# Kernel optimization log

Measured on AMD Instinct MI355X. Metric: run time of the kernel, lower is better.

Reference implementation:

```python
import jax, jax.numpy as jnp
import numpy as np

D_MODEL, N_LAYERS, D_INNER, D_STATE, D_CONV, DT_RANK, NUM_CLASSES = 256, 4, 512, 16, 4, 16, 10
B, L = 8, 1024


def setup_inputs() -> dict:
    key = jax.random.key(0)
    ks = jax.random.split(key, 16)
    s = 0.02
    inp = {}
    inp['x'] = jax.random.normal(ks[0], (B, L, 1), jnp.float32)
    inp['input_w'] = jax.random.normal(ks[1], (D_MODEL, 1), jnp.float32) * s
    inp['input_b'] = jnp.zeros((D_MODEL,), jnp.float32)
    inp['ln_w'] = jnp.ones((N_LAYERS, D_MODEL), jnp.float32)
    inp['ln_b'] = jnp.zeros((N_LAYERS, D_MODEL), jnp.float32)
    inp['in_proj_w'] = jax.random.normal(ks[2], (N_LAYERS, 2 * D_INNER, D_MODEL), jnp.float32) * s
    inp['in_proj_b'] = jnp.zeros((N_LAYERS, 2 * D_INNER), jnp.float32)
    inp['conv_w'] = jax.random.normal(ks[3], (N_LAYERS, D_INNER, 1, D_CONV), jnp.float32) * 0.2
    inp['conv_b'] = jnp.zeros((N_LAYERS, D_INNER), jnp.float32)
    inp['x_proj_w'] = jax.random.normal(ks[4], (N_LAYERS, DT_RANK + 2 * D_STATE, D_INNER), jnp.float32) * s
    inp['dt_proj_w'] = jax.random.normal(ks[5], (N_LAYERS, D_INNER, DT_RANK), jnp.float32) * s
    inp['dt_proj_b'] = jax.random.normal(ks[6], (N_LAYERS, D_INNER), jnp.float32) * 0.1 - 4.0  # small softplus(dt)
    # canonical S4D-real init: A = [1..d_state] repeated over d_inner
    A = jnp.tile(jnp.arange(1, D_STATE + 1, dtype=jnp.float32)[None, :], (D_INNER, 1))
    inp['A_log'] = jnp.tile(jnp.log(A)[None], (N_LAYERS, 1, 1))
    inp['D'] = jnp.ones((N_LAYERS, D_INNER), jnp.float32)
    inp['out_proj_w'] = jax.random.normal(ks[7], (N_LAYERS, D_MODEL, D_INNER), jnp.float32) * s
    inp['out_proj_b'] = jnp.zeros((N_LAYERS, D_MODEL), jnp.float32)
    inp['norm_w'] = jnp.ones((D_MODEL,), jnp.float32)
    inp['norm_b'] = jnp.zeros((D_MODEL,), jnp.float32)
    inp['cls_w'] = jax.random.normal(ks[8], (NUM_CLASSES, D_MODEL), jnp.float32) * s
    inp['cls_b'] = jnp.zeros((NUM_CLASSES,), jnp.float32)
    return inp


def _layernorm(x, w, b, eps=1e-5):
    mu = jnp.mean(x, axis=-1, keepdims=True)
    var = jnp.mean(jnp.square(x - mu), axis=-1, keepdims=True)
    return (x - mu) * jax.lax.rsqrt(var + eps) * w + b


def _causal_depthwise_conv(u, w, b):
    # u: (B, L, D_inner), w: (D_inner, 1, K), causal padding K-1
    out = jax.lax.conv_general_dilated(
        u.transpose(0, 2, 1), w, window_strides=(1,), padding=[(D_CONV - 1, 0)],
        feature_group_count=D_INNER, dimension_numbers=('NCH', 'OIH', 'NCH'))
    return out.transpose(0, 2, 1) + b


def _selective_scan(u, delta, A, Bm, Cm, Dp):
    # u, delta: (B,L,Din); Bm, Cm: (B,L,N); A: (Din,N); Dp: (Din,)
    def step(h, inp):
        d_t, B_t, C_t, u_t = inp                       # (B,Din),(B,N),(B,N),(B,Din)
        dA = jnp.exp(d_t[:, :, None] * A)              # (B,Din,N)
        dBu = d_t[:, :, None] * B_t[:, None, :] * u_t[:, :, None]
        h = dA * h + dBu
        y = jnp.einsum('bdn,bn->bd', h, C_t)
        return h, y
    h0 = jnp.zeros((u.shape[0], D_INNER, D_STATE), u.dtype)
    xs = (delta.transpose(1, 0, 2), Bm.transpose(1, 0, 2), Cm.transpose(1, 0, 2), u.transpose(1, 0, 2))
    _, ys = jax.lax.scan(step, h0, xs)                 # ys: (L,B,Din)
    return ys.transpose(1, 0, 2) + u * Dp


def _mamba_layer(x, ln_w, ln_b, ipw, ipb, cw, cb, xpw, dtw, dtb, A_log, Dp, opw, opb):
    h = _layernorm(x, ln_w, ln_b)
    xz = jnp.einsum('bld,ed->ble', h, ipw) + ipb       # (B,L,2*Din)
    u, res = jnp.split(xz, 2, axis=-1)
    u = jax.nn.silu(_causal_depthwise_conv(u, cw, cb))
    x_dbl = jnp.einsum('bld,ed->ble', u, xpw)          # (B,L,dt_rank+2N)
    dt, Bm, Cm = jnp.split(x_dbl, [DT_RANK, DT_RANK + D_STATE], axis=-1)
    delta = jax.nn.softplus(jnp.einsum('blr,dr->bld', dt, dtw) + dtb)
    A = -jnp.exp(A_log)
    y = _selective_scan(u, delta, A, Bm, Cm, Dp)
    y = y * jax.nn.silu(res)
    return x + jnp.einsum('ble,de->bld', y, opw) + opb


def reference(x, input_w, input_b, ln_w, ln_b, in_proj_w, in_proj_b, conv_w, conv_b,
              x_proj_w, dt_proj_w, dt_proj_b, A_log, D, out_proj_w, out_proj_b,
              norm_w, norm_b, cls_w, cls_b):
    h = jnp.einsum('blc,dc->bld', x, input_w) + input_b   # (B,L,D_MODEL)
    for i in range(N_LAYERS):
        h = _mamba_layer(h, ln_w[i], ln_b[i], in_proj_w[i], in_proj_b[i], conv_w[i], conv_b[i],
                         x_proj_w[i], dt_proj_w[i], dt_proj_b[i], A_log[i], D[i],
                         out_proj_w[i], out_proj_b[i])
    h = _layernorm(h, norm_w, norm_b)
    pooled = jnp.mean(h, axis=1)                          # (B, D_MODEL)
    return jnp.einsum('bd,cd->bc', pooled, cls_w) + cls_b
```

## Files before the change

### kernel.cpp

```cpp
#include <hip/hip_runtime.h>
#include <hip/hip_bf16.h>
#include <math.h>

#define DM 256
#define NL 4
#define DI 512
#define DS 16
#define DC 4
#define DR 16
#define NC 10
#define NB 8
#define LL 1024
#define MR (NB*LL)
#define NCHUNK 64
#define CLEN 16

typedef __attribute__((ext_vector_type(4))) float f32x4;
typedef __attribute__((ext_vector_type(8))) short short8;

__device__ __forceinline__ float silu_f(float x) {
    return x * (1.0f / (1.0f + __expf(-x)));
}
__device__ __forceinline__ float bf2f(ushort v) {
    union { unsigned u; float f; } c; c.u = ((unsigned)v) << 16; return c.f;
}
__device__ __forceinline__ ushort f2bf(float f) {
    union { float f; unsigned u; } c; c.f = f;
    unsigned lsb = (c.u >> 16) & 1;
    return (ushort)((c.u + 0x7fffu + lsb) >> 16);
}
__device__ __forceinline__ void g2lds16(const void* g, void* l) {
    __builtin_amdgcn_global_load_lds((const __attribute__((address_space(1))) void*)g,
                                     (__attribute__((address_space(3))) void*)l, 16, 0, 0);
}

#define IPW_N (NL*2*DI*DM)
#define XPW_N (NL*64*DI)
#define OPW_N (NL*DM*DI)
__global__ __launch_bounds__(256) void convert_weights_kernel(
        const float* __restrict__ ipw, const float* __restrict__ xpw,
        const float* __restrict__ opw,
        ushort* __restrict__ ipw_b, ushort* __restrict__ xpw_b, ushort* __restrict__ opw_b) {
    int t = blockIdx.x * 256 + threadIdx.x;
    if (t < IPW_N) { ipw_b[t] = f2bf(ipw[t]); return; }
    t -= IPW_N;
    if (t < XPW_N) {
        int l = t >> 15, r = (t >> 9) & 63, k = t & 511;
        xpw_b[t] = (r < 48) ? f2bf(xpw[((size_t)l * 48 + r) * DI + k]) : (ushort)0;
        return;
    }
    t -= XPW_N;
    if (t < OPW_N) opw_b[t] = f2bf(opw[t]);
}

__global__ void input_proj_kernel(const float* __restrict__ x, const float* __restrict__ w,
                                  const float* __restrict__ b, float* __restrict__ h) {
    int t = blockIdx.x * 256 + threadIdx.x;
    if (t >= MR * DM) return;
    int d = t & (DM - 1);
    int m = t >> 8;
    h[t] = x[m] * w[d] + b[d];
}

__global__ __launch_bounds__(256) void layernorm_bf16_kernel(const float* __restrict__ in,
        const float* __restrict__ w, const float* __restrict__ b, ushort* __restrict__ out) {
    int row = blockIdx.x, t = threadIdx.x;
    float v = in[row * DM + t];
    float s = v, q = v * v;
#pragma unroll
    for (int o = 32; o >= 1; o >>= 1) { s += __shfl_xor(s, o); q += __shfl_xor(q, o); }
    __shared__ float red[8];
    int wid = t >> 6;
    if ((t & 63) == 0) { red[wid] = s; red[4 + wid] = q; }
    __syncthreads();
    s = red[0] + red[1] + red[2] + red[3];
    q = red[4] + red[5] + red[6] + red[7];
    float mu = s * (1.0f / DM);
    float var = q * (1.0f / DM) - mu * mu;
    float rs = rsqrtf(var + 1e-5f);
    out[row * DM + t] = f2bf((v - mu) * rs * w[t] + b[t]);
}

template<int BM, int BN, int WM, int WN, int MODE>
__global__ __launch_bounds__(256) void mfma_gemm_kernel(
        const ushort* __restrict__ A, int lda,
        const ushort* __restrict__ W,
        const float* __restrict__ bias,
        ushort* __restrict__ Cb, float* __restrict__ Cf, int ldc, int K) {
    constexpr int FM = BM / WM / 16;
    constexpr int FN = BN / WN / 16;
    __shared__ __align__(16) char smem[(BM + BN) * 128];
    const int tid = threadIdx.x;
    const int l = tid & 63, w = tid >> 6;
    const int wr = w / WN, wc = w % WN;
    const int bm = blockIdx.x * BM, bn = blockIdx.y * BN;
    const int ldw = K;

    f32x4 acc[FM][FN] = {};

    for (int k0 = 0; k0 < K; k0 += 64) {
#pragma unroll
        for (int i = 0; i < (BM * 128 / 16) / 256; i++) {
            int lin = (i * 256 + tid) * 16;
            int q = lin ^ (((lin >> 7) & 7) << 4);
            g2lds16(A + (size_t)(bm + (q >> 7)) * lda + k0 + ((q & 127) >> 1), smem + lin);
        }
#pragma unroll
        for (int i = 0; i < (BN * 128 / 16) / 256; i++) {
            int lin = (i * 256 + tid) * 16;
            int q = lin ^ (((lin >> 7) & 7) << 4);
            g2lds16(W + (size_t)(bn + (q >> 7)) * ldw + k0 + ((q & 127) >> 1),
                    smem + BM * 128 + lin);
        }
        __syncthreads();
        const int rl = l & 15;
        const int kb0 = ((l >> 4) << 3) * 2;
#pragma unroll
        for (int kk = 0; kk < 2; kk++) {
            short8 af[FM], bfr[FN];
#pragma unroll
            for (int m = 0; m < FM; m++) {
                int off = (wr * (BM / WM) + m * 16 + rl) * 128 + kk * 64 + kb0;
                off ^= ((off >> 7) & 7) << 4;
                af[m] = *(const short8*)(smem + off);
            }
#pragma unroll
            for (int n = 0; n < FN; n++) {
                int off = (wc * (BN / WN) + n * 16 + rl) * 128 + kk * 64 + kb0;
                off ^= ((off >> 7) & 7) << 4;
                bfr[n] = *(const short8*)(smem + BM * 128 + off);
            }
#pragma unroll
            for (int m = 0; m < FM; m++)
#pragma unroll
                for (int n = 0; n < FN; n++)
                    acc[m][n] = __builtin_amdgcn_mfma_f32_16x16x32_bf16(
                        af[m], bfr[n], acc[m][n], 0, 0, 0);
        }
        __syncthreads();
    }

    const int row0 = bm + wr * (BM / WM) + ((l >> 4) << 2);
    const int col0 = bn + wc * (BN / WN) + (l & 15);
#pragma unroll
    for (int m = 0; m < FM; m++) {
#pragma unroll
        for (int n = 0; n < FN; n++) {
            int col = col0 + n * 16;
            float bv = (MODE == 1) ? 0.f : bias[col];
#pragma unroll
            for (int r = 0; r < 4; r++) {
                size_t idx = (size_t)(row0 + m * 16 + r) * ldc + col;
                float v = acc[m][n][r];
                if (MODE == 0) Cb[idx] = f2bf(v + bv);
                else if (MODE == 1) Cf[idx] = v;
                else Cf[idx] += v + bv;
            }
        }
    }
}

__global__ __launch_bounds__(256) void conv_silu_kernel(const ushort* __restrict__ xz,
        const float* __restrict__ cw, const float* __restrict__ cb, ushort* __restrict__ u) {
    int t = blockIdx.x * 256 + threadIdx.x;
    int d8 = (t & 63) << 3;
    int m = t >> 6;
    int l = m & (LL - 1);
    const short8 zr = {0, 0, 0, 0, 0, 0, 0, 0};
    const size_t base = (size_t)m * 1024 + d8;
    short8 r3 = *(const short8*)(xz + base);
    short8 r2 = (l >= 1) ? *(const short8*)(xz + base - 1024) : zr;
    short8 r1 = (l >= 2) ? *(const short8*)(xz + base - 2048) : zr;
    short8 r0 = (l >= 3) ? *(const short8*)(xz + base - 3072) : zr;
    short8 o;
#pragma unroll
    for (int j = 0; j < 8; j++) {
        int d = d8 + j;
        float4 w4 = *reinterpret_cast<const float4*>(&cw[d * 4]);
        float a = cb[d] + w4.w * bf2f((ushort)r3[j]);
        a += w4.z * bf2f((ushort)r2[j]);
        a += w4.y * bf2f((ushort)r1[j]);
        a += w4.x * bf2f((ushort)r0[j]);
        o[j] = (short)f2bf(silu_f(a));
    }
    *(short8*)(u + (size_t)m * DI + d8) = o;
}

__global__ __launch_bounds__(256, 4) void scan_phase1_kernel(
        const ushort* __restrict__ u, const float* __restrict__ x_dbl,
        const float* __restrict__ A_log,
        const float* __restrict__ dtw, const float* __restrict__ dtb,
        float* __restrict__ sdv, float* __restrict__ Sbuf) {
    __shared__ __align__(16) float xs[CLEN * 64];
    const int tid = threadIdx.x;
    const int bc = blockIdx.x >> 1;
    const int d = ((blockIdx.x & 1) << 8) + tid;
    const int c = bc & (NCHUNK - 1);
    const int b = bc >> 6;
    const int m0 = b * LL + c * CLEN;
    *reinterpret_cast<float4*>(&xs[tid * 4]) =
        *reinterpret_cast<const float4*>(&x_dbl[(size_t)m0 * 64 + tid * 4]);

    float Aval[DS], h[DS], wreg[DR];
#pragma unroll
    for (int q = 0; q < 4; q++) {
        float4 a4 = *reinterpret_cast<const float4*>(&A_log[d * DS + q * 4]);
        Aval[q*4+0] = -__expf(a4.x); Aval[q*4+1] = -__expf(a4.y);
        Aval[q*4+2] = -__expf(a4.z); Aval[q*4+3] = -__expf(a4.w);
        float4 w4 = *reinterpret_cast<const float4*>(&dtw[d * DR + q * 4]);
        wreg[q*4] = w4.x; wreg[q*4+1] = w4.y; wreg[q*4+2] = w4.z; wreg[q*4+3] = w4.w;
    }
    float dbv = dtb[d];
#pragma unroll
    for (int n = 0; n < DS; n++) h[n] = 0.f;
    const ushort* up = u + (size_t)m0 * DI + d;
    float sd = 0.f;
    __syncthreads();
    float uv = bf2f(up[0]);
    for (int t = 0; t < CLEN; t++) {
        float uvn = (t + 1 < CLEN) ? bf2f(up[(size_t)(t + 1) * DI]) : 0.f;
        const float* xr = &xs[t * 64];
        float p0 = dbv, p1 = 0.f, p2 = 0.f, p3 = 0.f;
#pragma unroll
        for (int k = 0; k < 4; k++) {
            p0 += wreg[k] * xr[k];
            p1 += wreg[4 + k] * xr[4 + k];
            p2 += wreg[8 + k] * xr[8 + k];
            p3 += wreg[12 + k] * xr[12 + k];
        }
        float z = (p0 + p1) + (p2 + p3);
        float dv = (z > 20.0f) ? z : __logf(1.0f + __expf(z));
        sd += dv;
        float du = dv * uv;
#pragma unroll
        for (int n = 0; n < DS; n++) {
            float dA = __expf(dv * Aval[n]);
            h[n] = dA * h[n] + du * xr[16 + n];
        }
        uv = uvn;
    }
    size_t base = ((size_t)((b * NCHUNK + c) * DI + d)) * DS;
#pragma unroll
    for (int q = 0; q < 4; q++)
        *reinterpret_cast<float4*>(&Sbuf[base + q * 4]) =
            make_float4(h[q*4], h[q*4+1], h[q*4+2], h[q*4+3]);
    sdv[(b * NCHUNK + c) * DI + d] = sd;
}

__global__ __launch_bounds__(256) void scan_phase2_kernel(
        const float* __restrict__ sdv, const float* __restrict__ A_log,
        float* __restrict__ Sbuf) {
    int gid = blockIdx.x * 256 + threadIdx.x;
    int dn = gid & (DI * DS - 1);
    int b = gid >> 13;
    int n = dn & 15, d = dn >> 4;
    float Aval = -__expf(A_log[d * DS + n]);
    size_t idx0 = (size_t)b * NCHUNK * DI * DS + dn;
    const size_t stride = (size_t)DI * DS;
    int sb0 = b * NCHUNK * DI + d;
    float h = 0.f;
    float Sc = Sbuf[idx0];
    float sd = sdv[sb0];
    for (int c = 0; c < NCHUNK; c++) {
        size_t idx = idx0 + (size_t)c * stride;
        float Sn = 0.f, sdn = 0.f;
        if (c + 1 < NCHUNK) {
            Sn = Sbuf[idx + stride];
            sdn = sdv[sb0 + (c + 1) * DI];
        }
        float Pc = __expf(Aval * sd);
        Sbuf[idx] = h;
        h = Pc * h + Sc;
        Sc = Sn; sd = sdn;
    }
}

__global__ __launch_bounds__(256, 4) void scan_phase3_kernel(
        const ushort* __restrict__ u, const float* __restrict__ x_dbl,
        const float* __restrict__ A_log,
        const float* __restrict__ dtw, const float* __restrict__ dtb,
        const float* __restrict__ Dp, const float* __restrict__ Sbuf,
        const ushort* __restrict__ xz, ushort* __restrict__ y) {
    __shared__ __align__(16) float xs[CLEN * 64];
    const int tid = threadIdx.x;
    const int bc = blockIdx.x >> 1;
    const int d = ((blockIdx.x & 1) << 8) + tid;
    const int c = bc & (NCHUNK - 1);
    const int b = bc >> 6;
    const int m0 = b * LL + c * CLEN;
    *reinterpret_cast<float4*>(&xs[tid * 4]) =
        *reinterpret_cast<const float4*>(&x_dbl[(size_t)m0 * 64 + tid * 4]);

    float Aval[DS], h[DS], wreg[DR];
#pragma unroll
    for (int q = 0; q < 4; q++) {
        float4 a4 = *reinterpret_cast<const float4*>(&A_log[d * DS + q * 4]);
        Aval[q*4+0] = -__expf(a4.x); Aval[q*4+1] = -__expf(a4.y);
        Aval[q*4+2] = -__expf(a4.z); Aval[q*4+3] = -__expf(a4.w);
        float4 w4 = *reinterpret_cast<const float4*>(&dtw[d * DR + q * 4]);
        wreg[q*4] = w4.x; wreg[q*4+1] = w4.y; wreg[q*4+2] = w4.z; wreg[q*4+3] = w4.w;
    }
    float dbv = dtb[d];
    size_t base = ((size_t)((b * NCHUNK + c) * DI + d)) * DS;
#pragma unroll
    for (int q = 0; q < 4; q++) {
        float4 h4 = *reinterpret_cast<const float4*>(&Sbuf[base + q * 4]);
        h[q*4] = h4.x; h[q*4+1] = h4.y; h[q*4+2] = h4.z; h[q*4+3] = h4.w;
    }
    float Dval = Dp[d];
    const ushort* up = u + (size_t)m0 * DI + d;
    const ushort* rp = xz + (size_t)m0 * 1024 + 512 + d;
    ushort* yp = y + (size_t)m0 * DI + d;
    __syncthreads();
    float uv = bf2f(up[0]);
    float rv = bf2f(rp[0]);
    for (int t = 0; t < CLEN; t++) {
        float uvn = 0.f, rvn = 0.f;
        if (t + 1 < CLEN) {
            uvn = bf2f(up[(size_t)(t + 1) * DI]);
            rvn = bf2f(rp[(size_t)(t + 1) * 1024]);
        }
        const float* xr = &xs[t * 64];
        float p0 = dbv, p1 = 0.f, p2 = 0.f, p3 = 0.f;
#pragma unroll
        for (int k = 0; k < 4; k++) {
            p0 += wreg[k] * xr[k];
            p1 += wreg[4 + k] * xr[4 + k];
            p2 += wreg[8 + k] * xr[8 + k];
            p3 += wreg[12 + k] * xr[12 + k];
        }
        float z = (p0 + p1) + (p2 + p3);
        float dv = (z > 20.0f) ? z : __logf(1.0f + __expf(z));
        float du = dv * uv;
        float a0 = 0.f, a1 = 0.f, a2 = 0.f, a3 = 0.f;
#pragma unroll
        for (int j = 0; j < 4; j++) {
            {
                int n = j;
                float dA = __expf(dv * Aval[n]);
                h[n] = dA * h[n] + du * xr[16 + n];
                a0 += h[n] * xr[32 + n];
            }
            {
                int n = 4 + j;
                float dA = __expf(dv * Aval[n]);
                h[n] = dA * h[n] + du * xr[16 + n];
                a1 += h[n] * xr[32 + n];
            }
            {
                int n = 8 + j;
                float dA = __expf(dv * Aval[n]);
                h[n] = dA * h[n] + du * xr[16 + n];
                a2 += h[n] * xr[32 + n];
            }
            {
                int n = 12 + j;
                float dA = __expf(dv * Aval[n]);
                h[n] = dA * h[n] + du * xr[16 + n];
                a3 += h[n] * xr[32 + n];
            }
        }
        float acc = ((a0 + a1) + (a2 + a3)) + Dval * uv;
        yp[(size_t)t * DI] = f2bf(acc * silu_f(rv));
        uv = uvn; rv = rvn;
    }
}

__global__ __launch_bounds__(256) void pool_partial_kernel(const ushort* __restrict__ ln,
                                                           float* __restrict__ partial) {
    int bs = blockIdx.x;
    int b = bs >> 3, sl = bs & 7;
    int t = threadIdx.x;
    int l0 = sl * 128;
    float s = 0.f;
    for (int l = 0; l < 128; l++) s += bf2f(ln[(size_t)(b * LL + l0 + l) * DM + t]);
    partial[(bs << 8) + t] = s;
}

__global__ void cls_kernel(const float* __restrict__ partial, const float* __restrict__ cw,
                           const float* __restrict__ cb, float* __restrict__ out) {
    int t = threadIdx.x;
    if (t >= NB * NC) return;
    int b = t / NC, c = t % NC;
    float s = 0.f;
    for (int k = 0; k < DM; k++) {
        float p = 0.f;
#pragma unroll
        for (int sl = 0; sl < 8; sl++) p += partial[((b * 8 + sl) << 8) + k];
        s += p * cw[c * DM + k];
    }
    out[t] = cb[c] + s * (1.0f / LL);
}

extern "C" void kernel_launch(void* const* d_in, const int* in_sizes, int n_in,
                              void* d_out, int out_size, void* d_ws, size_t ws_size,
                              hipStream_t stream) {
    const float* x       = (const float*)d_in[0];
    const float* input_w = (const float*)d_in[1];
    const float* input_b = (const float*)d_in[2];
    const float* ln_w    = (const float*)d_in[3];
    const float* ln_b    = (const float*)d_in[4];
    const float* ipw     = (const float*)d_in[5];
    const float* ipb     = (const float*)d_in[6];
    const float* cw      = (const float*)d_in[7];
    const float* cb      = (const float*)d_in[8];
    const float* xpw     = (const float*)d_in[9];
    const float* dtw     = (const float*)d_in[10];
    const float* dtb     = (const float*)d_in[11];
    const float* A_log   = (const float*)d_in[12];
    const float* Dp      = (const float*)d_in[13];
    const float* opw     = (const float*)d_in[14];
    const float* opb     = (const float*)d_in[15];
    const float* norm_w  = (const float*)d_in[16];
    const float* norm_b  = (const float*)d_in[17];
    const float* cls_w   = (const float*)d_in[18];
    const float* cls_b   = (const float*)d_in[19];
    float* out = (float*)d_out;
    float* ws = (float*)d_ws;

    float*  hres   = ws;
    ushort* xz     = (ushort*)(hres + (size_t)MR * DM);
    ushort* ub     = xz + (size_t)MR * 1024;
    float*  x_dbl  = (float*)(ub + (size_t)MR * DI);
    float*  sdvb   = x_dbl + (size_t)MR * 64;
    float*  Sbuf   = sdvb + (size_t)NB * NCHUNK * DI;
    float*  partial= Sbuf + (size_t)NB * NCHUNK * DI * DS;
    ushort* ygate  = (ushort*)(partial + 64 * 256);
    ushort* hln    = ygate + (size_t)MR * DI;
    ushort* ipw_b  = hln + (size_t)MR * DM;
    ushort* xpw_b  = ipw_b + IPW_N;
    ushort* opw_b  = xpw_b + XPW_N;

    convert_weights_kernel<<<(IPW_N + XPW_N + OPW_N) / 256, 256, 0, stream>>>(
        ipw, xpw, opw, ipw_b, xpw_b, opw_b);
    input_proj_kernel<<<MR * DM / 256, 256, 0, stream>>>(x, input_w, input_b, hres);

    for (int i = 0; i < NL; i++) {
        layernorm_bf16_kernel<<<MR, 256, 0, stream>>>(hres, ln_w + i * DM, ln_b + i * DM, hln);
        mfma_gemm_kernel<128, 128, 2, 2, 0><<<dim3(MR / 128, 1024 / 128), 256, 0, stream>>>(
            hln, DM, ipw_b + (size_t)i * 2 * DI * DM, ipb + (size_t)i * 2 * DI,
            xz, nullptr, 1024, DM);
        conv_silu_kernel<<<MR * DI / 8 / 256, 256, 0, stream>>>(xz, cw + i * DI * DC, cb + i * DI, ub);
        mfma_gemm_kernel<64, 64, 4, 1, 1><<<dim3(MR / 64, 1), 256, 0, stream>>>(
            ub, DI, xpw_b + (size_t)i * 64 * DI, nullptr, nullptr, x_dbl, 64, DI);
        scan_phase1_kernel<<<NB * NCHUNK * DI / 256, 256, 0, stream>>>(
            ub, x_dbl, A_log + i * DI * DS, dtw + i * DI * DR, dtb + i * DI, sdvb, Sbuf);
        scan_phase2_kernel<<<NB * DI * DS / 256, 256, 0, stream>>>(
            sdvb, A_log + i * DI * DS, Sbuf);
        scan_phase3_kernel<<<NB * NCHUNK * DI / 256, 256, 0, stream>>>(
            ub, x_dbl, A_log + i * DI * DS, dtw + i * DI * DR, dtb + i * DI,
            Dp + i * DI, Sbuf, xz, ygate);
        mfma_gemm_kernel<64, 128, 2, 2, 2><<<dim3(MR / 64, DM / 128), 256, 0, stream>>>(
            ygate, DI, opw_b + (size_t)i * DM * DI, opb + (size_t)i * DM,
            nullptr, hres, DM, DI);
    }

    layernorm_bf16_kernel<<<MR, 256, 0, stream>>>(hres, norm_w, norm_b, hln);
    pool_partial_kernel<<<64, 256, 0, stream>>>(hln, partial);
    cls_kernel<<<1, 128, 0, stream>>>(partial, cls_w, cls_b, out);
}
```

Before: 503.1 us.

## Parallelize chunk-state scan with warp shuffle scan and retile x_proj GEMM

Phase 2 of the selective scan previously ran a serial loop over 64 chunks per (b,d,n) thread. It now stages 16 channels' chunk states into shared memory and runs a log-step warp-shuffle associative scan across chunks, writing exclusive prefix states back. Block count stays at 256, but each thread now handles 64 independent short scans instead of one 64-step dependent chain, which removes the serial dependency latency. The x_proj GEMM also switches to 32-row tiles, doubling its block count for better occupancy at the cost of less weight reuse per block.

```diff
diff --git a/kernel.cpp b/kernel.cpp
--- a/kernel.cpp
+++ b/kernel.cpp
@@ -250,28 +250,46 @@
 __global__ __launch_bounds__(256) void scan_phase2_kernel(
         const float* __restrict__ sdv, const float* __restrict__ A_log,
         float* __restrict__ Sbuf) {
-    int gid = blockIdx.x * 256 + threadIdx.x;
-    int dn = gid & (DI * DS - 1);
-    int b = gid >> 13;
-    int n = dn & 15, d = dn >> 4;
-    float Aval = -__expf(A_log[d * DS + n]);
-    size_t idx0 = (size_t)b * NCHUNK * DI * DS + dn;
-    const size_t stride = (size_t)DI * DS;
-    int sb0 = b * NCHUNK * DI + d;
-    float h = 0.f;
-    float Sc = Sbuf[idx0];
-    float sd = sdv[sb0];
-    for (int c = 0; c < NCHUNK; c++) {
-        size_t idx = idx0 + (size_t)c * stride;
-        float Sn = 0.f, sdn = 0.f;
-        if (c + 1 < NCHUNK) {
-            Sn = Sbuf[idx + stride];
-            sdn = sdv[sb0 + (c + 1) * DI];
-        }
-        float Pc = __expf(Aval * sd);
-        Sbuf[idx] = h;
-        h = Pc * h + Sc;
-        Sc = Sn; sd = sdn;
+    __shared__ float L[256][65];
+    __shared__ float sdvL[16][64];
+    __shared__ float AvalL[256];
+    const int t = threadIdx.x;
+    const int b = blockIdx.x >> 5;
+    const int d0 = (blockIdx.x & 31) << 4;
+    {
+        const float* src = Sbuf + ((size_t)(b * NCHUNK) * DI + d0) * DS + t;
+        for (int c = 0; c < NCHUNK; c++)
+            L[t][c] = src[(size_t)c * DI * DS];
+    }
+    {
+        int c = t >> 2, i0 = (t & 3) << 2;
+        float4 v = *reinterpret_cast<const float4*>(
+            &sdv[(size_t)(b * NCHUNK + c) * DI + d0 + i0]);
+        sdvL[i0 + 0][c] = v.x; sdvL[i0 + 1][c] = v.y;
+        sdvL[i0 + 2][c] = v.z; sdvL[i0 + 3][c] = v.w;
+    }
+    AvalL[t] = -__expf(A_log[(d0 + (t >> 4)) * DS + (t & 15)]);
+    __syncthreads();
+    const int lane = t & 63, w = t >> 6;
+    for (int j = 0; j < 64; j++) {
+        int dn = w * 64 + j;
+        float S = L[dn][lane];
+        float P = __expf(AvalL[dn] * sdvL[dn >> 4][lane]);
+#pragma unroll
+        for (int off = 1; off < 64; off <<= 1) {
+            float Pp = __shfl_up(P, off);
+            float Sp = __shfl_up(S, off);
+            if (lane >= off) { S = P * Sp + S; P = P * Pp; }
+        }
+        float hin = __shfl_up(S, 1);
+        if (lane == 0) hin = 0.f;
+        L[dn][lane] = hin;
+    }
+    __syncthreads();
+    {
+        float* dst = Sbuf + ((size_t)(b * NCHUNK) * DI + d0) * DS + t;
+        for (int c = 0; c < NCHUNK; c++)
+            dst[(size_t)c * DI * DS] = L[t][c];
     }
 }
 
@@ -441,11 +459,11 @@
             hln, DM, ipw_b + (size_t)i * 2 * DI * DM, ipb + (size_t)i * 2 * DI,
             xz, nullptr, 1024, DM);
         conv_silu_kernel<<<MR * DI / 8 / 256, 256, 0, stream>>>(xz, cw + i * DI * DC, cb + i * DI, ub);
-        mfma_gemm_kernel<64, 64, 4, 1, 1><<<dim3(MR / 64, 1), 256, 0, stream>>>(
+        mfma_gemm_kernel<32, 64, 2, 2, 1><<<dim3(MR / 32, 1), 256, 0, stream>>>(
             ub, DI, xpw_b + (size_t)i * 64 * DI, nullptr, nullptr, x_dbl, 64, DI);
         scan_phase1_kernel<<<NB * NCHUNK * DI / 256, 256, 0, stream>>>(
             ub, x_dbl, A_log + i * DI * DS, dtw + i * DI * DR, dtb + i * DI, sdvb, Sbuf);
-        scan_phase2_kernel<<<NB * DI * DS / 256, 256, 0, stream>>>(
+        scan_phase2_kernel<<<NB * (DI / 16), 256, 0, stream>>>(
             sdvb, A_log + i * DI * DS, Sbuf);
         scan_phase3_kernel<<<NB * NCHUNK * DI / 256, 256, 0, stream>>>(
             ub, x_dbl, A_log + i * DI * DS, dtw + i * DI * DR, dtb + i * DI,
```

Result: slower. 566.4 us (+12.6%).
